# Kernel tuning notes

Measured on AMD Instinct MI355X. Metric: run time of the kernel, lower is better.

Reference implementation:

```python
import jax, jax.numpy as jnp
import numpy as np

C = 64          # hidden width fixed by DirModel
N_BLOCKS = 5    # five DirResNet2 blocks
EPS = 1e-5      # BatchNorm eps (torch default)


def graph_bn(x, gamma, beta):
    # GraphBatchNorm: BatchNorm1d over flattened (B*N, C), training-mode batch stats
    m = x.mean(axis=(0, 1))
    var = ((x - m) ** 2).mean(axis=(0, 1))  # biased variance, as torch BN uses
    return (x - m) * jax.lax.rsqrt(var + EPS) * gamma + beta


def graph_conv1x1_pre(x, W, b, gamma, beta):
    # GraphConv1x1 with batch_norm='pre': BN then per-node Linear
    return graph_bn(x, gamma, beta) @ W + b


def dir_resnet2(Di, DiA, v, f, W0, b0, g0, be0, W1, b1, g1, be1):
    # Quaternion Dirac message passing: C feats = C//4 quaternion channels.
    B, N, Cv = v.shape
    Fc = f.shape[1]
    q = Cv // 4
    # vertex -> face
    x = jax.nn.elu(v)
    x = graph_conv1x1_pre(x, W0, b0, g0, be0)
    x = jax.nn.elu(x)
    f_new = jnp.matmul(Di, x.reshape(B, 4 * N, q)).reshape(B, Fc, Cv)  # Di:[B,4F,4N]
    f = f + f_new
    # face -> vertex (adjoint)
    y = jax.nn.elu(f)
    y = graph_conv1x1_pre(y, W1, b1, g1, be1)
    y = jax.nn.elu(y)
    v_new = jnp.matmul(DiA, y.reshape(B, 4 * Fc, q)).reshape(B, N, Cv)  # DiA:[B,4N,4F]
    v = v + v_new
    return v, f


def setup_inputs() -> dict:
    key = jax.random.key(0)
    ks = jax.random.split(key, 24)
    B, N, Fc = 2, 1024, 2048
    inputs = jax.random.normal(ks[0], (B, N, 3), dtype=jnp.float32)
    # dense incidence operators (scaled to keep activations tame over 5 blocks)
    Di = jax.random.normal(ks[1], (B, 4 * Fc, 4 * N), dtype=jnp.float32) * 0.05
    DiA = jax.random.normal(ks[2], (B, 4 * N, 4 * Fc), dtype=jnp.float32) * 0.05
    mask = jnp.ones((B, N, 1), dtype=jnp.float32)
    p = {}
    p['W_in'] = jax.random.normal(ks[3], (3, C), dtype=jnp.float32) * 0.05
    p['b_in'] = jnp.zeros((C,), jnp.float32)
    p['rn_W0'] = jax.random.normal(ks[4], (N_BLOCKS, C, C), dtype=jnp.float32) * 0.05
    p['rn_b0'] = jnp.zeros((N_BLOCKS, C), jnp.float32)
    p['rn_g0'] = jnp.ones((N_BLOCKS, C), jnp.float32)
    p['rn_be0'] = jnp.zeros((N_BLOCKS, C), jnp.float32)
    p['rn_W1'] = jax.random.normal(ks[5], (N_BLOCKS, C, C), dtype=jnp.float32) * 0.05
    p['rn_b1'] = jnp.zeros((N_BLOCKS, C), jnp.float32)
    p['rn_g1'] = jnp.ones((N_BLOCKS, C), jnp.float32)
    p['rn_be1'] = jnp.zeros((N_BLOCKS, C), jnp.float32)
    p['bn2_g'] = jnp.ones((C,), jnp.float32)
    p['bn2_b'] = jnp.zeros((C,), jnp.float32)
    p['W2'] = jax.random.normal(ks[6], (C, C), dtype=jnp.float32) * 0.05
    p['b2'] = jnp.zeros((C,), jnp.float32)
    p['Wfc'] = jax.random.normal(ks[7], (C, 10), dtype=jnp.float32) * 0.05
    p['bfc'] = jnp.zeros((10,), jnp.float32)
    return dict(inputs=inputs, Di=Di, DiA=DiA, mask=mask, **p)


def reference(inputs, Di, DiA, mask, W_in, b_in, rn_W0, rn_b0, rn_g0, rn_be0,
              rn_W1, rn_b1, rn_g1, rn_be1, bn2_g, bn2_b, W2, b2, Wfc, bfc):
    B, N, _ = inputs.shape
    v = inputs @ W_in + b_in                       # conv1 (no BN)
    Fc = DiA.shape[2] // 4
    f = jnp.zeros((B, Fc, C), inputs.dtype)
    for i in range(N_BLOCKS):                      # fixed small loop over blocks
        v, f = dir_resnet2(Di, DiA, v, f,
                           rn_W0[i], rn_b0[i], rn_g0[i], rn_be0[i],
                           rn_W1[i], rn_b1[i], rn_g1[i], rn_be1[i])
    v = jax.nn.elu(v)
    v = graph_conv1x1_pre(v, W2, b2, bn2_g, bn2_b)  # bn_conv2
    v = jax.nn.elu(v)
    pooled = (v * mask).sum(axis=1) / mask.sum(axis=1)  # masked global average -> [B, C]
    logits = pooled @ Wfc + bfc                    # dropout is identity in eval
    return jax.nn.log_softmax(logits, axis=-1)
```

## Files before the change

kernel.cpp:

```cpp
#include <hip/hip_runtime.h>
#include <math.h>

#define EPSBN 1e-5f

typedef __fp16 h2 __attribute__((ext_vector_type(2)));
typedef __attribute__((address_space(1))) const void gv_t;
typedef __attribute__((address_space(3))) void lv_t;

__device__ inline unsigned pkrtz(float a, float b) {
  h2 r = __builtin_amdgcn_cvt_pkrtz(a, b);
  return __builtin_bit_cast(unsigned, r);
}

#if defined(__has_builtin) && __has_builtin(__builtin_amdgcn_fdot2)
__device__ inline float dot2(unsigned a, unsigned b, float c) {
  return __builtin_amdgcn_fdot2(__builtin_bit_cast(h2, a),
                                __builtin_bit_cast(h2, b), c, false);
}
#else
__device__ inline float dot2(unsigned a, unsigned b, float c) {
  h2 ha = __builtin_bit_cast(h2, a), hb = __builtin_bit_cast(h2, b);
  return c + (float)ha[0] * (float)hb[0] + (float)ha[1] * (float)hb[1];
}
#endif

__device__ inline void stage16(const unsigned short* g, unsigned short* l, int lane) {
#if defined(__has_builtin) && __has_builtin(__builtin_amdgcn_global_load_lds)
  __builtin_amdgcn_global_load_lds((gv_t*)(g + lane * 8), (lv_t*)l, 16, 0, 0);
#else
  *(uint4*)(l + lane * 8) = *(const uint4*)(g + lane * 8);
#endif
}

__device__ inline float eluf(float x) { return x > 0.f ? x : expm1f(x); }

__global__ void k_in(const float* __restrict__ inp, const float* __restrict__ Win,
                     const float* __restrict__ bin, float* __restrict__ v, int total) {
  int g = blockIdx.x * 256 + threadIdx.x;
  if (g >= total) return;
  int row = g >> 6, c = g & 63;
  float s = bin[c] + inp[row * 3 + 0] * Win[c] + inp[row * 3 + 1] * Win[64 + c] +
            inp[row * 3 + 2] * Win[128 + c];
  v[g] = s;
}

__global__ void k_stats(const float* __restrict__ z, float* __restrict__ part, int R) {
  __shared__ float s1s[4][64], s2s[4][64];
  int c = threadIdx.x & 63, g = threadIdx.x >> 6;
  float s1 = 0.f, s2 = 0.f;
  for (int row = blockIdx.x * 4 + g; row < R; row += 256) {
    float t = eluf(z[row * 64 + c]);
    s1 += t; s2 += t * t;
  }
  s1s[g][c] = s1; s2s[g][c] = s2;
  __syncthreads();
  if (threadIdx.x < 64) {
    part[blockIdx.x * 128 + c] = s1s[0][c] + s1s[1][c] + s1s[2][c] + s1s[3][c];
    part[blockIdx.x * 128 + 64 + c] = s2s[0][c] + s2s[1][c] + s2s[2][c] + s2s[3][c];
  }
}

__global__ void k_transform(const float* __restrict__ z, const float* __restrict__ part,
                            const float* __restrict__ gamma, const float* __restrict__ beta,
                            const float* __restrict__ W, const float* __restrict__ bias,
                            unsigned short* __restrict__ Xt, int R, int Kx) {
  __shared__ float Wl[64][65];
  __shared__ float ab[2][64];
  __shared__ float xn[4][64];
  int tid = threadIdx.x, c = tid & 63, ns = tid >> 6;
  if (tid < 64) {
    float s1 = 0.f, s2 = 0.f;
    for (int g2 = 0; g2 < 64; ++g2) {
      s1 += part[g2 * 128 + tid];
      s2 += part[g2 * 128 + 64 + tid];
    }
    float m = s1 / (float)R;
    float var = s2 / (float)R - m * m;
    float a = gamma[tid] * rsqrtf(var + EPSBN);
    ab[0][tid] = a; ab[1][tid] = beta[tid] - m * a;
  }
  for (int i = tid; i < 4096; i += 256) Wl[i >> 6][i & 63] = W[i];
  __syncthreads();
  int rpb = R >> 1;
  for (int rowg = blockIdx.x; rowg * 4 < R; rowg += gridDim.x) {
    int row = rowg * 4 + ns;
    float t = eluf(z[row * 64 + c]);
    xn[ns][c] = t * ab[0][c] + ab[1][c];
    __syncthreads();
    float acc = bias[c];
#pragma unroll
    for (int d = 0; d < 64; ++d) acc += xn[ns][d] * Wl[d][c];
    float o = eluf(acc);
    int b = row >= rpb ? 1 : 0;
    int n = row - b * rpb;
    _Float16 oh = (_Float16)o;
    Xt[(size_t)b * 16 * Kx + (size_t)(c & 15) * Kx + 4 * n + (c >> 4)] =
        __builtin_bit_cast(unsigned short, oh);
    __syncthreads();
  }
}

template <int MODE>
__global__ __launch_bounds__(256, 4) void k_bigmat(const float* __restrict__ Df,
                                                   unsigned short* __restrict__ D16,
                                                   const unsigned short* __restrict__ Xt,
                                                   float* __restrict__ out, int M, int K) {
  __shared__ __align__(16) unsigned char smem[33792];
  unsigned short* xs = (unsigned short*)smem;
  int tid = threadIdx.x;
  int wv = tid >> 6, lane = tid & 63;
  int b = blockIdx.y;
  size_t bstr = (size_t)M * (size_t)K;
  const float* df = Df + (size_t)b * bstr;
  unsigned short* d16 = D16 + (MODE == 0 ? 0 : (size_t)b * bstr);
  const unsigned short* xg = Xt + (size_t)b * 16 * K;
  float* ob = out + (size_t)b * M * 16;
  int row0 = blockIdx.x * 16 + wv * 4;

  float acc[4][16];
#pragma unroll
  for (int r = 0; r < 4; r++) {
#pragma unroll
    for (int j = 0; j < 16; j++) acc[r][j] = 0.f;
  }
  const int nc = K >> 9;

  auto stage = [&](int buf, int chunk) {
    unsigned short* base = xs + buf * (16 * 520);
#pragma unroll
    for (int q = 0; q < 4; q++) {
      int j = wv * 4 + q;
      const unsigned short* g = xg + (size_t)j * K + chunk * 512;
      stage16(g, base + j * 520, lane);
    }
  };

  stage(0, 0);
  __syncthreads();
  for (int c = 0; c < nc; ++c) {
    if (c + 1 < nc) stage((c + 1) & 1, c + 1);
    const unsigned short* xb = xs + (c & 1) * (16 * 520);
    uint4 d[4];
#pragma unroll
    for (int r = 0; r < 4; r++) {
      size_t off = (size_t)(row0 + r) * K + c * 512 + lane * 8;
      if (MODE == 2) {
        d[r] = *(const uint4*)(d16 + off);
      } else {
        const float4 a = *(const float4*)(df + off);
        const float4 bb = *(const float4*)(df + off + 4);
        d[r].x = pkrtz(a.x, a.y); d[r].y = pkrtz(a.z, a.w);
        d[r].z = pkrtz(bb.x, bb.y); d[r].w = pkrtz(bb.z, bb.w);
        if (MODE == 1) *(uint4*)(d16 + off) = d[r];
      }
    }
#pragma unroll
    for (int j = 0; j < 16; j++) {
      const uint4 x = *(const uint4*)(xb + j * 520 + lane * 8);
#pragma unroll
      for (int r = 0; r < 4; r++) {
        acc[r][j] = dot2(d[r].x, x.x, acc[r][j]);
        acc[r][j] = dot2(d[r].y, x.y, acc[r][j]);
        acc[r][j] = dot2(d[r].z, x.z, acc[r][j]);
        acc[r][j] = dot2(d[r].w, x.w, acc[r][j]);
      }
    }
    __syncthreads();
  }

  float* red = (float*)smem + wv * 2112;
#pragma unroll
  for (int t = 0; t < 2; t++) {
#pragma unroll
    for (int i = 0; i < 32; i++) red[lane * 33 + i] = acc[2 * t + (i >> 4)][i & 15];
    float s = 0.f;
    int ci = lane & 31, pb = (lane >> 5) * 32;
#pragma unroll
    for (int p = 0; p < 32; p++) s += red[(pb + p) * 33 + ci];
    s += __shfl_xor(s, 32);
    if (lane < 32) {
      int r = 2 * t + (lane >> 4), j = lane & 15;
      ob[(size_t)(row0 + r) * 16 + j] += s;
    }
  }
}

__global__ void k_trans_pool(const float* __restrict__ z, const float* __restrict__ part,
                             const float* __restrict__ gamma, const float* __restrict__ beta,
                             const float* __restrict__ W, const float* __restrict__ bias,
                             const float* __restrict__ mask, float* __restrict__ pp) {
  const int R = 2048;
  __shared__ float Wl[64][65];
  __shared__ float ab[2][64];
  __shared__ float xn[4][64];
  __shared__ float rr[4][128];
  int tid = threadIdx.x, c = tid & 63, ns = tid >> 6;
  if (tid < 64) {
    float s1 = 0.f, s2 = 0.f;
    for (int g2 = 0; g2 < 64; ++g2) {
      s1 += part[g2 * 128 + tid];
      s2 += part[g2 * 128 + 64 + tid];
    }
    float m = s1 / (float)R;
    float var = s2 / (float)R - m * m;
    float a = gamma[tid] * rsqrtf(var + EPSBN);
    ab[0][tid] = a; ab[1][tid] = beta[tid] - m * a;
  }
  for (int i = tid; i < 4096; i += 256) Wl[i >> 6][i & 63] = W[i];
  __syncthreads();
  float po0 = 0.f, po1 = 0.f;
  for (int rowg = blockIdx.x; rowg * 4 < R; rowg += gridDim.x) {
    int row = rowg * 4 + ns;
    float t = eluf(z[row * 64 + c]);
    xn[ns][c] = t * ab[0][c] + ab[1][c];
    __syncthreads();
    float acc = bias[c];
#pragma unroll
    for (int d = 0; d < 64; ++d) acc += xn[ns][d] * Wl[d][c];
    float o = eluf(acc) * mask[row];
    if (row < 1024) po0 += o; else po1 += o;
    __syncthreads();
  }
  rr[ns][c] = po0; rr[ns][64 + c] = po1;
  __syncthreads();
  if (tid < 128)
    pp[blockIdx.x * 128 + tid] = rr[0][tid] + rr[1][tid] + rr[2][tid] + rr[3][tid];
}

__global__ void k_final(const float* __restrict__ pp, const float* __restrict__ mask,
                        const float* __restrict__ Wfc, const float* __restrict__ bfc,
                        float* __restrict__ outp) {
  __shared__ float pooled[128];
  __shared__ float msum[2];
  __shared__ float lg[20];
  __shared__ float msr[256];
  int tid = threadIdx.x;
  {
    int b2 = tid >> 7, st = tid & 127;
    float s = 0.f;
    for (int n = st; n < 1024; n += 128) s += mask[b2 * 1024 + n];
    msr[tid] = s;
  }
  __syncthreads();
  if (tid < 2) {
    float s = 0.f;
    for (int i = 0; i < 128; i++) s += msr[tid * 128 + i];
    msum[tid] = s;
  }
  __syncthreads();
  if (tid < 128) {
    float s = 0.f;
    for (int g = 0; g < 128; ++g) s += pp[g * 128 + tid];
    pooled[tid] = s / msum[tid >> 6];
  }
  __syncthreads();
  if (tid < 20) {
    int b2 = tid / 10, o = tid % 10;
    float s = bfc[o];
    for (int c2 = 0; c2 < 64; ++c2) s += pooled[b2 * 64 + c2] * Wfc[c2 * 10 + o];
    lg[tid] = s;
  }
  __syncthreads();
  if (tid < 2) {
    float m = -1e30f;
    for (int o = 0; o < 10; o++) m = fmaxf(m, lg[tid * 10 + o]);
    float se = 0.f;
    for (int o = 0; o < 10; o++) se += expf(lg[tid * 10 + o] - m);
    float ls = m + logf(se);
    for (int o = 0; o < 10; o++) outp[tid * 10 + o] = lg[tid * 10 + o] - ls;
  }
}

extern "C" void kernel_launch(void* const* d_in, const int* in_sizes, int n_in,
                              void* d_out, int out_size, void* d_ws, size_t ws_size,
                              hipStream_t stream) {
  (void)in_sizes; (void)n_in; (void)out_size;
  const float* inp  = (const float*)d_in[0];
  const float* Di   = (const float*)d_in[1];
  const float* DiA  = (const float*)d_in[2];
  const float* mask = (const float*)d_in[3];
  const float* Win  = (const float*)d_in[4];
  const float* bin  = (const float*)d_in[5];
  const float* W0   = (const float*)d_in[6];
  const float* b0   = (const float*)d_in[7];
  const float* g0   = (const float*)d_in[8];
  const float* be0  = (const float*)d_in[9];
  const float* W1   = (const float*)d_in[10];
  const float* b1   = (const float*)d_in[11];
  const float* g1   = (const float*)d_in[12];
  const float* be1  = (const float*)d_in[13];
  const float* g2   = (const float*)d_in[14];
  const float* be2  = (const float*)d_in[15];
  const float* W2   = (const float*)d_in[16];
  const float* b2   = (const float*)d_in[17];
  const float* Wfc  = (const float*)d_in[18];
  const float* bfc  = (const float*)d_in[19];
  float* outp = (float*)d_out;

  const size_t d16Bytes = 2ULL * 8192 * 4096 * 2;
  bool f16ok = ws_size >= (2 * d16Bytes + 4ULL * 1024 * 1024);
  char* wsB = (char*)d_ws;
  size_t off = f16ok ? 2 * d16Bytes : 0;
  unsigned short* Di16  = (unsigned short*)wsB;
  unsigned short* DiA16 = (unsigned short*)(wsB + d16Bytes);
  float* v = (float*)(wsB + off);            off += 2ULL * 1024 * 64 * 4;
  float* f = (float*)(wsB + off);            off += 2ULL * 2048 * 64 * 4;
  unsigned short* Xt = (unsigned short*)(wsB + off); off += 2ULL * 16 * 8192 * 2;
  float* part = (float*)(wsB + off);         off += 64 * 128 * 4;
  float* pp = (float*)(wsB + off);           off += 128 * 128 * 4;

  (void)hipMemsetAsync(f, 0, 2ULL * 2048 * 64 * 4, stream);
  k_in<<<512, 256, 0, stream>>>(inp, Win, bin, v, 131072);
  for (int i = 0; i < 5; i++) {
    k_stats<<<64, 256, 0, stream>>>(v, part, 2048);
    k_transform<<<128, 256, 0, stream>>>(v, part, g0 + i * 64, be0 + i * 64,
                                         W0 + i * 4096, b0 + i * 64, Xt, 2048, 4096);
    if (!f16ok)
      k_bigmat<0><<<dim3(512, 2), 256, 0, stream>>>(Di, Di16, Xt, f, 8192, 4096);
    else if (i == 0)
      k_bigmat<1><<<dim3(512, 2), 256, 0, stream>>>(Di, Di16, Xt, f, 8192, 4096);
    else
      k_bigmat<2><<<dim3(512, 2), 256, 0, stream>>>(Di, Di16, Xt, f, 8192, 4096);

    k_stats<<<64, 256, 0, stream>>>(f, part, 4096);
    k_transform<<<128, 256, 0, stream>>>(f, part, g1 + i * 64, be1 + i * 64,
                                         W1 + i * 4096, b1 + i * 64, Xt, 4096, 8192);
    if (!f16ok)
      k_bigmat<0><<<dim3(256, 2), 256, 0, stream>>>(DiA, DiA16, Xt, v, 4096, 8192);
    else if (i == 0)
      k_bigmat<1><<<dim3(256, 2), 256, 0, stream>>>(DiA, DiA16, Xt, v, 4096, 8192);
    else
      k_bigmat<2><<<dim3(256, 2), 256, 0, stream>>>(DiA, DiA16, Xt, v, 4096, 8192);
  }
  k_stats<<<64, 256, 0, stream>>>(v, part, 2048);
  k_trans_pool<<<128, 256, 0, stream>>>(v, part, g2, be2, W2, b2, mask, pp);
  k_final<<<1, 256, 0, stream>>>(pp, mask, Wfc, bfc, outp);
}
```

Measured before the change: 1.105 ms.

## Fuse BatchNorm statistics into producer kernels and drop separate stats launches

Moves the ELU+sum/sum-of-squares batch statistics into the epilogues of k_in and k_bigmat, accumulating with atomics into 32 partial slots. This removes all k_stats launches and their extra pass over v and f. The first Di matmul now writes f directly instead of needing a memset, and bigmat zeroes the other stats buffer for the next stage. k_transform keeps the weight column in registers instead of LDS, reads activations as float4, and launches with more blocks. The cost is atomic contention on the stats slots and higher register pressure in the transform kernels.

```diff
diff --git a/kernel.cpp b/kernel.cpp
--- a/kernel.cpp
+++ b/kernel.cpp
@@ -35,61 +35,66 @@
 __device__ inline float eluf(float x) { return x > 0.f ? x : expm1f(x); }
 
 __global__ void k_in(const float* __restrict__ inp, const float* __restrict__ Win,
-                     const float* __restrict__ bin, float* __restrict__ v, int total) {
-  int g = blockIdx.x * 256 + threadIdx.x;
-  if (g >= total) return;
-  int row = g >> 6, c = g & 63;
+                     const float* __restrict__ bin, float* __restrict__ v,
+                     float* __restrict__ pv) {
+  __shared__ float s1s[4][64], s2s[4][64];
+  int tid = threadIdx.x;
+  int g = blockIdx.x * 256 + tid;
+  int row = g >> 6, c = g & 63, ns = tid >> 6;
   float s = bin[c] + inp[row * 3 + 0] * Win[c] + inp[row * 3 + 1] * Win[64 + c] +
             inp[row * 3 + 2] * Win[128 + c];
   v[g] = s;
-}
-
-__global__ void k_stats(const float* __restrict__ z, float* __restrict__ part, int R) {
-  __shared__ float s1s[4][64], s2s[4][64];
-  int c = threadIdx.x & 63, g = threadIdx.x >> 6;
-  float s1 = 0.f, s2 = 0.f;
-  for (int row = blockIdx.x * 4 + g; row < R; row += 256) {
-    float t = eluf(z[row * 64 + c]);
-    s1 += t; s2 += t * t;
-  }
-  s1s[g][c] = s1; s2s[g][c] = s2;
-  __syncthreads();
-  if (threadIdx.x < 64) {
-    part[blockIdx.x * 128 + c] = s1s[0][c] + s1s[1][c] + s1s[2][c] + s1s[3][c];
-    part[blockIdx.x * 128 + 64 + c] = s2s[0][c] + s2s[1][c] + s2s[2][c] + s2s[3][c];
-  }
-}
-
-__global__ void k_transform(const float* __restrict__ z, const float* __restrict__ part,
-                            const float* __restrict__ gamma, const float* __restrict__ beta,
-                            const float* __restrict__ W, const float* __restrict__ bias,
-                            unsigned short* __restrict__ Xt, int R, int Kx) {
-  __shared__ float Wl[64][65];
+  float e = eluf(s);
+  s1s[ns][c] = e; s2s[ns][c] = e * e;
+  __syncthreads();
+  if (tid < 128) {
+    int c2 = tid & 63;
+    float t = (tid < 64) ? s1s[0][c2] + s1s[1][c2] + s1s[2][c2] + s1s[3][c2]
+                         : s2s[0][c2] + s2s[1][c2] + s2s[2][c2] + s2s[3][c2];
+    atomicAdd(&pv[(blockIdx.x & 31) * 128 + tid], t);
+  }
+}
+
+__global__ __launch_bounds__(256) void k_transform(
+    const float* __restrict__ z, const float* __restrict__ part,
+    const float* __restrict__ gamma, const float* __restrict__ beta,
+    const float* __restrict__ W, const float* __restrict__ bias,
+    unsigned short* __restrict__ Xt, int R, int Kx) {
   __shared__ float ab[2][64];
   __shared__ float xn[4][64];
+  __shared__ float red[128];
   int tid = threadIdx.x, c = tid & 63, ns = tid >> 6;
+  float wc[64];
+#pragma unroll
+  for (int d = 0; d < 64; ++d) wc[d] = W[d * 64 + c];
+  if (tid < 128) {
+    float s = 0.f;
+#pragma unroll
+    for (int g2 = 0; g2 < 32; ++g2) s += part[g2 * 128 + tid];
+    red[tid] = s;
+  }
+  __syncthreads();
   if (tid < 64) {
-    float s1 = 0.f, s2 = 0.f;
-    for (int g2 = 0; g2 < 64; ++g2) {
-      s1 += part[g2 * 128 + tid];
-      s2 += part[g2 * 128 + 64 + tid];
-    }
-    float m = s1 / (float)R;
-    float var = s2 / (float)R - m * m;
+    float m = red[tid] / (float)R;
+    float var = red[64 + tid] / (float)R - m * m;
     float a = gamma[tid] * rsqrtf(var + EPSBN);
     ab[0][tid] = a; ab[1][tid] = beta[tid] - m * a;
   }
-  for (int i = tid; i < 4096; i += 256) Wl[i >> 6][i & 63] = W[i];
-  __syncthreads();
+  __syncthreads();
+  float biasc = bias[c];
   int rpb = R >> 1;
   for (int rowg = blockIdx.x; rowg * 4 < R; rowg += gridDim.x) {
     int row = rowg * 4 + ns;
     float t = eluf(z[row * 64 + c]);
     xn[ns][c] = t * ab[0][c] + ab[1][c];
     __syncthreads();
-    float acc = bias[c];
-#pragma unroll
-    for (int d = 0; d < 64; ++d) acc += xn[ns][d] * Wl[d][c];
+    float acc = biasc;
+#pragma unroll
+    for (int d4 = 0; d4 < 16; ++d4) {
+      float4 xv = *(const float4*)&xn[ns][d4 * 4];
+      acc += xv.x * wc[4 * d4] + xv.y * wc[4 * d4 + 1] + xv.z * wc[4 * d4 + 2] +
+             xv.w * wc[4 * d4 + 3];
+    }
     float o = eluf(acc);
     int b = row >= rpb ? 1 : 0;
     int n = row - b * rpb;
@@ -100,14 +105,19 @@
   }
 }
 
-template <int MODE>
+template <int MODE, int ZERO>
 __global__ __launch_bounds__(256, 4) void k_bigmat(const float* __restrict__ Df,
                                                    unsigned short* __restrict__ D16,
                                                    const unsigned short* __restrict__ Xt,
-                                                   float* __restrict__ out, int M, int K) {
+                                                   float* __restrict__ out, int M, int K,
+                                                   float* __restrict__ statp,
+                                                   float* __restrict__ zbuf) {
   __shared__ __align__(16) unsigned char smem[33792];
+  __shared__ float st1[4][64], st2[4][64];
   unsigned short* xs = (unsigned short*)smem;
   int tid = threadIdx.x;
+  if (tid < 128 && blockIdx.y == 0 && blockIdx.x < 32)
+    zbuf[blockIdx.x * 128 + tid] = 0.f;
   int wv = tid >> 6, lane = tid & 63;
   int b = blockIdx.y;
   size_t bstr = (size_t)M * (size_t)K;
@@ -180,8 +190,20 @@
     s += __shfl_xor(s, 32);
     if (lane < 32) {
       int r = 2 * t + (lane >> 4), j = lane & 15;
-      ob[(size_t)(row0 + r) * 16 + j] += s;
-    }
+      size_t oi = (size_t)(row0 + r) * 16 + j;
+      float val = ZERO ? s : ob[oi] + s;
+      ob[oi] = val;
+      float e = eluf(val);
+      int ch = ((r & 3) << 4) | j;
+      st1[wv][ch] = e; st2[wv][ch] = e * e;
+    }
+  }
+  __syncthreads();
+  if (tid < 128) {
+    int c2 = tid & 63;
+    float t2 = (tid < 64) ? st1[0][c2] + st1[1][c2] + st1[2][c2] + st1[3][c2]
+                          : st2[0][c2] + st2[1][c2] + st2[2][c2] + st2[3][c2];
+    atomicAdd(&statp[(blockIdx.x & 31) * 128 + tid], t2);
   }
 }
 
@@ -190,33 +212,42 @@
                              const float* __restrict__ W, const float* __restrict__ bias,
                              const float* __restrict__ mask, float* __restrict__ pp) {
   const int R = 2048;
-  __shared__ float Wl[64][65];
   __shared__ float ab[2][64];
   __shared__ float xn[4][64];
   __shared__ float rr[4][128];
+  __shared__ float red[128];
   int tid = threadIdx.x, c = tid & 63, ns = tid >> 6;
+  float wc[64];
+#pragma unroll
+  for (int d = 0; d < 64; ++d) wc[d] = W[d * 64 + c];
+  if (tid < 128) {
+    float s = 0.f;
+#pragma unroll
+    for (int g2 = 0; g2 < 32; ++g2) s += part[g2 * 128 + tid];
+    red[tid] = s;
+  }
+  __syncthreads();
   if (tid < 64) {
-    float s1 = 0.f, s2 = 0.f;
-    for (int g2 = 0; g2 < 64; ++g2) {
-      s1 += part[g2 * 128 + tid];
-      s2 += part[g2 * 128 + 64 + tid];
-    }
-    float m = s1 / (float)R;
-    float var = s2 / (float)R - m * m;
+    float m = red[tid] / (float)R;
+    float var = red[64 + tid] / (float)R - m * m;
     float a = gamma[tid] * rsqrtf(var + EPSBN);
     ab[0][tid] = a; ab[1][tid] = beta[tid] - m * a;
   }
-  for (int i = tid; i < 4096; i += 256) Wl[i >> 6][i & 63] = W[i];
-  __syncthreads();
+  __syncthreads();
+  float biasc = bias[c];
   float po0 = 0.f, po1 = 0.f;
   for (int rowg = blockIdx.x; rowg * 4 < R; rowg += gridDim.x) {
     int row = rowg * 4 + ns;
     float t = eluf(z[row * 64 + c]);
     xn[ns][c] = t * ab[0][c] + ab[1][c];
     __syncthreads();
-    float acc = bias[c];
-#pragma unroll
-    for (int d = 0; d < 64; ++d) acc += xn[ns][d] * Wl[d][c];
+    float acc = biasc;
+#pragma unroll
+    for (int d4 = 0; d4 < 16; ++d4) {
+      float4 xv = *(const float4*)&xn[ns][d4 * 4];
+      acc += xv.x * wc[4 * d4] + xv.y * wc[4 * d4 + 1] + xv.z * wc[4 * d4 + 2] +
+             xv.w * wc[4 * d4 + 3];
+    }
     float o = eluf(acc) * mask[row];
     if (row < 1024) po0 += o; else po1 += o;
     __syncthreads();
@@ -306,33 +337,36 @@
   float* v = (float*)(wsB + off);            off += 2ULL * 1024 * 64 * 4;
   float* f = (float*)(wsB + off);            off += 2ULL * 2048 * 64 * 4;
   unsigned short* Xt = (unsigned short*)(wsB + off); off += 2ULL * 16 * 8192 * 2;
-  float* part = (float*)(wsB + off);         off += 64 * 128 * 4;
+  float* pv = (float*)(wsB + off);           off += 32 * 128 * 4;
+  float* pf = (float*)(wsB + off);           off += 32 * 128 * 4;
   float* pp = (float*)(wsB + off);           off += 128 * 128 * 4;
 
-  (void)hipMemsetAsync(f, 0, 2ULL * 2048 * 64 * 4, stream);
-  k_in<<<512, 256, 0, stream>>>(inp, Win, bin, v, 131072);
+  (void)hipMemsetAsync(pv, 0, 2 * 32 * 128 * 4, stream);
+  k_in<<<512, 256, 0, stream>>>(inp, Win, bin, v, pv);
   for (int i = 0; i < 5; i++) {
-    k_stats<<<64, 256, 0, stream>>>(v, part, 2048);
-    k_transform<<<128, 256, 0, stream>>>(v, part, g0 + i * 64, be0 + i * 64,
+    k_transform<<<512, 256, 0, stream>>>(v, pv, g0 + i * 64, be0 + i * 64,
                                          W0 + i * 4096, b0 + i * 64, Xt, 2048, 4096);
-    if (!f16ok)
-      k_bigmat<0><<<dim3(512, 2), 256, 0, stream>>>(Di, Di16, Xt, f, 8192, 4096);
-    else if (i == 0)
-      k_bigmat<1><<<dim3(512, 2), 256, 0, stream>>>(Di, Di16, Xt, f, 8192, 4096);
-    else
-      k_bigmat<2><<<dim3(512, 2), 256, 0, stream>>>(Di, Di16, Xt, f, 8192, 4096);
-
-    k_stats<<<64, 256, 0, stream>>>(f, part, 4096);
-    k_transform<<<128, 256, 0, stream>>>(f, part, g1 + i * 64, be1 + i * 64,
+    if (!f16ok) {
+      if (i == 0)
+        k_bigmat<0, 1><<<dim3(512, 2), 256, 0, stream>>>(Di, Di16, Xt, f, 8192, 4096, pf, pv);
+      else
+        k_bigmat<0, 0><<<dim3(512, 2), 256, 0, stream>>>(Di, Di16, Xt, f, 8192, 4096, pf, pv);
+    } else if (i == 0) {
+      k_bigmat<1, 1><<<dim3(512, 2), 256, 0, stream>>>(Di, Di16, Xt, f, 8192, 4096, pf, pv);
+    } else {
+      k_bigmat<2, 0><<<dim3(512, 2), 256, 0, stream>>>(Di, Di16, Xt, f, 8192, 4096, pf, pv);
+    }
+
+    k_transform<<<512, 256, 0, stream>>>(f, pf, g1 + i * 64, be1 + i * 64,
                                          W1 + i * 4096, b1 + i * 64, Xt, 4096, 8192);
-    if (!f16ok)
-      k_bigmat<0><<<dim3(256, 2), 256, 0, stream>>>(DiA, DiA16, Xt, v, 4096, 8192);
-    else if (i == 0)
-      k_bigmat<1><<<dim3(256, 2), 256, 0, stream>>>(DiA, DiA16, Xt, v, 4096, 8192);
-    else
-      k_bigmat<2><<<dim3(256, 2), 256, 0, stream>>>(DiA, DiA16, Xt, v, 4096, 8192);
-  }
-  k_stats<<<64, 256, 0, stream>>>(v, part, 2048);
-  k_trans_pool<<<128, 256, 0, stream>>>(v, part, g2, be2, W2, b2, mask, pp);
+    if (!f16ok) {
+      k_bigmat<0, 0><<<dim3(256, 2), 256, 0, stream>>>(DiA, DiA16, Xt, v, 4096, 8192, pv, pf);
+    } else if (i == 0) {
+      k_bigmat<1, 0><<<dim3(256, 2), 256, 0, stream>>>(DiA, DiA16, Xt, v, 4096, 8192, pv, pf);
+    } else {
+      k_bigmat<2, 0><<<dim3(256, 2), 256, 0, stream>>>(DiA, DiA16, Xt, v, 4096, 8192, pv, pf);
+    }
+  }
+  k_trans_pool<<<128, 256, 0, stream>>>(v, pv, g2, be2, W2, b2, mask, pp);
   k_final<<<1, 256, 0, stream>>>(pp, mask, Wfc, bfc, outp);
 }
```

After: 982.4 us. -11.1%, faster.
